# Kernel optimization log

Measured on AMD Instinct MI355X. Metric: run time of the kernel, lower is better.

The kernel has to match this reference:

```python
import jax, jax.numpy as jnp
import numpy as np

N_ATOMS = 50000
N_EDGES = 1_600_000
H = 128
EPS = 1e-3  # keras BatchNormalization default epsilon


def _bn(x, gamma, beta, mean, var):
    # inference-mode batch norm with moving statistics
    return gamma * (x - mean) * jax.lax.rsqrt(var + EPS) + beta


def setup_inputs() -> dict:
    key = jax.random.key(0)
    ks = jax.random.split(key, 16)
    s = 0.05
    D1 = H + 1
    inp = {
        "atom_embedding": jax.random.normal(ks[0], (N_ATOMS, H), jnp.float32),
        "bond_embedding": jax.random.normal(ks[1], (N_EDGES, H), jnp.float32),
        "indices_i": jax.random.randint(ks[2], (N_EDGES,), 0, N_ATOMS, dtype=jnp.int32),
        "indices_j": jax.random.randint(ks[3], (N_EDGES,), 0, N_ATOMS, dtype=jnp.int32),
        # preprocess: Dense(3H -> H+1, no bias) + BN, Dense(H+1 -> H+1, no bias) + BN
        "W1": jax.random.normal(ks[4], (3 * H, D1), jnp.float32) * s,
        "g1": jnp.ones((D1,), jnp.float32),
        "b1": jnp.zeros((D1,), jnp.float32),
        "m1": jnp.zeros((D1,), jnp.float32),
        "v1": jnp.ones((D1,), jnp.float32),
        "W2": jax.random.normal(ks[5], (D1, D1), jnp.float32) * s,
        "g2": jnp.ones((D1,), jnp.float32),
        "b2": jnp.zeros((D1,), jnp.float32),
        "m2": jnp.zeros((D1,), jnp.float32),
        "v2": jnp.ones((D1,), jnp.float32),
        # two residual layers, each: x + (x@w1+b1)@w2+b2 (activation=None)
        "r1w1": jax.random.normal(ks[6], (H, H), jnp.float32) * s,
        "r1b1": jnp.zeros((H,), jnp.float32),
        "r1w2": jax.random.normal(ks[7], (H, H), jnp.float32) * s,
        "r1b2": jnp.zeros((H,), jnp.float32),
        "r2w1": jax.random.normal(ks[8], (H, H), jnp.float32) * s,
        "r2b1": jnp.zeros((H,), jnp.float32),
        "r2w2": jax.random.normal(ks[9], (H, H), jnp.float32) * s,
        "r2b2": jnp.zeros((H,), jnp.float32),
    }
    return inp


def reference(atom_embedding, bond_embedding, indices_i, indices_j,
              W1, g1, b1, m1, v1, W2, g2, b2, m2, v2,
              r1w1, r1b1, r1w2, r1b2, r2w1, r2b1, r2w2, r2b2):
    # gather endpoints: [E, H]
    ai = atom_embedding[indices_i]
    aj = atom_embedding[indices_j]
    x = jnp.concatenate([ai, bond_embedding, aj], axis=-1)  # [E, 3H]
    x = _bn(x @ W1, g1, b1, m1, v1)  # [E, H+1]
    x = _bn(x @ W2, g2, b2, m2, v2)  # [E, H+1]
    msg = x[:, :1] * x[:, 1:]  # gate * message -> [E, H]
    atom = atom_embedding + jax.ops.segment_sum(msg, indices_i, num_segments=N_ATOMS)
    # residual MLPs (activation=None -> identity)
    atom = atom + (atom @ r1w1 + r1b1) @ r1w2 + r1b2
    atom = atom + (atom @ r2w1 + r2b1) @ r2w2 + r2b2
    return atom
```

## Files before the change

### kernel.cpp

```cpp
#include <hip/hip_runtime.h>

#define NA 50000
#define NE 1600000
#define HH 128
#define D1 129
#define EPS 1e-3f

typedef __bf16 bf16_t;
typedef bf16_t bf16x8 __attribute__((ext_vector_type(8)));
typedef bf16_t bf16x4 __attribute__((ext_vector_type(4)));
typedef float f32x4 __attribute__((ext_vector_type(4)));

#define OFF_A1   0
#define OFF_C1   129
#define OFF_A2   258
#define OFF_C2   387
#define OFF_WEFF 516
#define OFF_DVEC (OFF_WEFF + 384*129)
#define OFF_Q1   (OFF_DVEC + 129)
#define OFF_Q2   (OFF_Q1 + 128*128)
#define OFF_q1   (OFF_Q2 + 128*128)
#define OFF_q2   (OFF_q1 + 128)
#define OFF_QF   (OFF_q2 + 128)
#define OFF_qf   (OFF_QF + 128*128)
#define OFF_WMT  (((OFF_qf + 128) + 3) & ~3)
#define OFF_WTT  (OFF_WMT + 9216)
#define OFF_WBT  (OFF_WTT + 9216)
#define OFF_QFT  (OFF_WBT + 9216)
#define OFF_PI   (OFF_QFT + 8192)
#define OFF_PJ   (OFF_PI + NA*D1)
#define OFF_ACC  (OFF_PJ + NA*D1)
#define OFF_ACC2 (OFF_ACC + NA*HH)
#define OFF_CNT  (OFF_ACC2 + NA)
#define OFF_CUR  (OFF_CNT + NA)
#define OFF_EDG  (OFF_CUR + NA)
#define OFF_PART (OFF_EDG + NE)
#define OFF_IIS  (OFF_PART + 256)
#define OFF_JJS  (OFF_IIS + NE)
#define SCAN_NB  ((NA + 255) / 256)

__global__ void k_affine(const float* __restrict__ g1, const float* __restrict__ b1,
                         const float* __restrict__ m1, const float* __restrict__ v1,
                         const float* __restrict__ g2, const float* __restrict__ b2,
                         const float* __restrict__ m2, const float* __restrict__ v2,
                         float* __restrict__ ws) {
    for (int idx = threadIdx.x; idx < 2 * D1; idx += blockDim.x) {
        if (idx < D1) {
            float a = g1[idx] * rsqrtf(v1[idx] + EPS);
            ws[OFF_A1 + idx] = a;
            ws[OFF_C1 + idx] = b1[idx] - m1[idx] * a;
        } else {
            int n = idx - D1;
            float a = g2[n] * rsqrtf(v2[n] + EPS);
            ws[OFF_A2 + n] = a;
            ws[OFF_C2 + n] = b2[n] - m2[n] * a;
        }
    }
}

__global__ void k_weff(const float* __restrict__ W1, const float* __restrict__ W2,
                       float* __restrict__ ws) {
    int idx = blockIdx.x * blockDim.x + threadIdx.x;
    if (idx >= 384 * D1 + D1) return;
    const float* a1 = ws + OFF_A1;
    const float* c1 = ws + OFF_C1;
    const float* a2 = ws + OFF_A2;
    const float* c2 = ws + OFF_C2;
    if (idx < 384 * D1) {
        int k = idx / D1, n = idx % D1;
        float s = 0.f;
        for (int t = 0; t < D1; ++t)
            s += W1[(size_t)k * D1 + t] * a1[t] * W2[(size_t)t * D1 + n];
        ws[OFF_WEFF + idx] = s * a2[n];
    } else {
        int n = idx - 384 * D1;
        float s = 0.f;
        for (int t = 0; t < D1; ++t)
            s += c1[t] * W2[(size_t)t * D1 + n];
        ws[OFF_DVEC + n] = s * a2[n] + c2[n];
    }
}

__global__ void k_resid(const float* __restrict__ r1w1, const float* __restrict__ r1b1,
                        const float* __restrict__ r1w2, const float* __restrict__ r1b2,
                        const float* __restrict__ r2w1, const float* __restrict__ r2b1,
                        const float* __restrict__ r2w2, const float* __restrict__ r2b2,
                        float* __restrict__ ws) {
    int idx = blockIdx.x * blockDim.x + threadIdx.x;
    if (idx >= 2 * (128 * 128 + 128)) return;
    int layer = idx / (128 * 128 + 128);
    int r = idx % (128 * 128 + 128);
    const float* w1 = layer ? r2w1 : r1w1;
    const float* b1 = layer ? r2b1 : r1b1;
    const float* w2 = layer ? r2w2 : r1w2;
    const float* b2 = layer ? r2b2 : r1b2;
    float* Q = ws + (layer ? OFF_Q2 : OFF_Q1);
    float* q = ws + (layer ? OFF_q2 : OFF_q1);
    if (r < 128 * 128) {
        int i = r >> 7, j = r & 127;
        float s = (i == j) ? 1.f : 0.f;
        for (int t = 0; t < 128; ++t)
            s += w1[i * 128 + t] * w2[t * 128 + j];
        Q[r] = s;
    } else {
        int j = r - 128 * 128;
        float s = b2[j];
        for (int t = 0; t < 128; ++t)
            s += b1[t] * w2[t * 128 + j];
        q[j] = s;
    }
}

__global__ void k_qf(float* __restrict__ ws) {
    int idx = blockIdx.x * blockDim.x + threadIdx.x;
    if (idx >= 128 * 128 + 128) return;
    const float* Q1 = ws + OFF_Q1;
    const float* Q2 = ws + OFF_Q2;
    if (idx < 128 * 128) {
        int i = idx >> 7, j = idx & 127;
        float s = 0.f;
        for (int m = 0; m < 128; ++m)
            s += Q1[i * 128 + m] * Q2[m * 128 + j];
        ws[OFF_QF + idx] = s;
    } else {
        int j = idx - 128 * 128;
        const float* q1 = ws + OFF_q1;
        float s = ws[OFF_q2 + j];
        for (int m = 0; m < 128; ++m)
            s += q1[m] * Q2[m * 128 + j];
        ws[OFF_qf + j] = s;
    }
}

__global__ void k_pack(float* __restrict__ ws) {
    int idx = blockIdx.x * blockDim.x + threadIdx.x;
    const float* Weff = ws + OFF_WEFF;
    if (idx < 18432) {
        int n = idx >> 7, k = idx & 127;
        float v = (n < 128) ? Weff[(size_t)(128 + k) * D1 + n + 1]
                            : ((n == 128) ? Weff[(size_t)(128 + k) * D1] : 0.f);
        ((bf16_t*)(ws + OFF_WMT))[idx] = (bf16_t)v;
    } else if (idx < 2 * 18432) {
        int r = idx - 18432;
        int n = r >> 7, k = r & 127;
        float v = (n < D1) ? Weff[(size_t)k * D1 + n] : 0.f;
        ((bf16_t*)(ws + OFF_WTT))[r] = (bf16_t)v;
    } else if (idx < 3 * 18432) {
        int r = idx - 2 * 18432;
        int n = r >> 7, k = r & 127;
        float v = (n < D1) ? Weff[(size_t)(256 + k) * D1 + n] : 0.f;
        ((bf16_t*)(ws + OFF_WBT))[r] = (bf16_t)v;
    } else if (idx < 3 * 18432 + 16384) {
        int r = idx - 3 * 18432;
        int n = r >> 7, k = r & 127;
        ((bf16_t*)(ws + OFF_QFT))[r] = (bf16_t)ws[OFF_QF + k * 128 + n];
    }
}

__global__ void k_hist(const int* __restrict__ idx_i, float* __restrict__ ws) {
    int e = blockIdx.x * blockDim.x + threadIdx.x;
    if (e < NE) atomicAdd((int*)(ws + OFF_CNT) + idx_i[e], 1);
}

__global__ void k_scan1(float* __restrict__ ws) {
    const int* cnt = (const int*)(ws + OFF_CNT);
    int i = blockIdx.x * 256 + threadIdx.x;
    int v = (i < NA) ? cnt[i] : 0;
#pragma unroll
    for (int o = 1; o < 64; o <<= 1) v += __shfl_xor(v, o);
    __shared__ int wsum[4];
    if ((threadIdx.x & 63) == 0) wsum[threadIdx.x >> 6] = v;
    __syncthreads();
    if (threadIdx.x == 0)
        ((int*)(ws + OFF_PART))[blockIdx.x] = wsum[0] + wsum[1] + wsum[2] + wsum[3];
}

__global__ void k_scan2(float* __restrict__ ws) {
    int* part = (int*)(ws + OFF_PART);
    __shared__ int ps[256];
    int t = threadIdx.x;
    int v = (t < SCAN_NB) ? part[t] : 0;
    ps[t] = v;
    __syncthreads();
    for (int o = 1; o < 256; o <<= 1) {
        int u = (t >= o) ? ps[t - o] : 0;
        __syncthreads();
        ps[t] += u;
        __syncthreads();
    }
    part[t] = t ? ps[t - 1] : 0;
}

__global__ void k_scan3(float* __restrict__ ws) {
    const int* cnt = (const int*)(ws + OFF_CNT);
    int* cursor = (int*)(ws + OFF_CUR);
    int base = ((const int*)(ws + OFF_PART))[blockIdx.x];
    int i = blockIdx.x * 256 + threadIdx.x;
    int v = (i < NA) ? cnt[i] : 0;
    int lane = threadIdx.x & 63, w = threadIdx.x >> 6;
    int s = v;
#pragma unroll
    for (int o = 1; o < 64; o <<= 1) {
        int u = __shfl_up(s, o);
        if (lane >= o) s += u;
    }
    __shared__ int wtot[4];
    if (lane == 63) wtot[w] = s;
    __syncthreads();
    int add = 0;
    for (int k = 0; k < 4; ++k)
        if (k < w) add += wtot[k];
    if (i < NA) cursor[i] = base + add + s - v;
}

__global__ void k_scatter(const int* __restrict__ idx_i, const int* __restrict__ idx_j,
                          float* __restrict__ ws) {
    int e = blockIdx.x * blockDim.x + threadIdx.x;
    if (e < NE) {
        int i = idx_i[e];
        int p = atomicAdd((int*)(ws + OFF_CUR) + i, 1);
        ((int*)(ws + OFF_EDG))[p] = e;
        ((int*)(ws + OFF_IIS))[p] = i;
        ((int*)(ws + OFF_JJS))[p] = idx_j[e];
    }
}

__global__ __launch_bounds__(256) void k_gemm_mfma(
    const float* __restrict__ A, const float* __restrict__ A2,
    const float* __restrict__ Pi, const float* __restrict__ acc2,
    const bf16_t* __restrict__ Wt, const float* __restrict__ bias,
    float* __restrict__ C, int ldc, int N, int ntiles, int M) {
    __shared__ __align__(16) bf16_t As[64][136];
    int t = threadIdx.x;
    int m0 = blockIdx.x * 64;
#pragma unroll
    for (int it = 0; it < 8; ++it) {
        int idx = t + 256 * it;
        int r = idx >> 5, c4 = idx & 31;
        int grow = m0 + r;
        float4 v = make_float4(0.f, 0.f, 0.f, 0.f);
        if (grow < M) {
            v = ((const float4*)(A + (size_t)grow * 128))[c4];
            if (A2) {
                float4 w = ((const float4*)(A2 + (size_t)grow * 128))[c4];
                v.x += w.x; v.y += w.y; v.z += w.z; v.w += w.w;
            }
            if (acc2) {
                float s = acc2[grow];
                const float* p = Pi + (size_t)grow * D1 + 1 + c4 * 4;
                v.x += s * p[0]; v.y += s * p[1]; v.z += s * p[2]; v.w += s * p[3];
            }
        }
        bf16x4 tmp;
        tmp[0] = (bf16_t)v.x; tmp[1] = (bf16_t)v.y; tmp[2] = (bf16_t)v.z; tmp[3] = (bf16_t)v.w;
        *(bf16x4*)&As[r][c4 * 4] = tmp;
    }
    __syncthreads();
    int lane = t & 63, w = t >> 6;
    int ll = lane & 15, quad = lane >> 4;
    bf16x8 a[4];
#pragma unroll
    for (int k = 0; k < 4; ++k)
        a[k] = *(const bf16x8*)&As[w * 16 + ll][k * 32 + quad * 8];
    for (int nt = 0; nt < ntiles; ++nt) {
        const bf16_t* bp = Wt + (size_t)(nt * 16 + ll) * 128 + quad * 8;
        f32x4 acc = {0.f, 0.f, 0.f, 0.f};
#pragma unroll
        for (int k = 0; k < 4; ++k) {
            bf16x8 b = *(const bf16x8*)(bp + k * 32);
            acc = __builtin_amdgcn_mfma_f32_16x16x32_bf16(a[k], b, acc, 0, 0, 0);
        }
        int col = nt * 16 + ll;
        if (col < N) {
            float bv = bias ? bias[col] : 0.f;
#pragma unroll
            for (int r = 0; r < 4; ++r) {
                int row = m0 + w * 16 + quad * 4 + r;
                if (row < M) C[(size_t)row * ldc + col] = acc[r] + bv;
            }
        }
    }
}

__global__ __launch_bounds__(256) void k_pipj(
    const float* __restrict__ A, const bf16_t* __restrict__ Wt,
    const float* __restrict__ bias, float* __restrict__ Ct,
    const bf16_t* __restrict__ Wb, float* __restrict__ Cb, int M) {
    __shared__ __align__(16) bf16_t As[64][136];
    int t = threadIdx.x;
    int m0 = blockIdx.x * 64;
#pragma unroll
    for (int it = 0; it < 8; ++it) {
        int idx = t + 256 * it;
        int r = idx >> 5, c4 = idx & 31;
        int grow = m0 + r;
        float4 v = make_float4(0.f, 0.f, 0.f, 0.f);
        if (grow < M) v = ((const float4*)(A + (size_t)grow * 128))[c4];
        bf16x4 tmp;
        tmp[0] = (bf16_t)v.x; tmp[1] = (bf16_t)v.y; tmp[2] = (bf16_t)v.z; tmp[3] = (bf16_t)v.w;
        *(bf16x4*)&As[r][c4 * 4] = tmp;
    }
    __syncthreads();
    int lane = t & 63, w = t >> 6;
    int ll = lane & 15, quad = lane >> 4;
    bf16x8 a[4];
#pragma unroll
    for (int k = 0; k < 4; ++k)
        a[k] = *(const bf16x8*)&As[w * 16 + ll][k * 32 + quad * 8];
    for (int half = 0; half < 2; ++half) {
        const bf16_t* W = half ? Wb : Wt;
        float* C = half ? Cb : Ct;
        for (int nt = 0; nt < 9; ++nt) {
            const bf16_t* bp = W + (size_t)(nt * 16 + ll) * 128 + quad * 8;
            f32x4 acc = {0.f, 0.f, 0.f, 0.f};
#pragma unroll
            for (int k = 0; k < 4; ++k) {
                bf16x8 b = *(const bf16x8*)(bp + k * 32);
                acc = __builtin_amdgcn_mfma_f32_16x16x32_bf16(a[k], b, acc, 0, 0, 0);
            }
            int col = nt * 16 + ll;
            if (col < D1) {
                float bv = (half == 0 && bias) ? bias[col] : 0.f;
#pragma unroll
                for (int r = 0; r < 4; ++r) {
                    int row = m0 + w * 16 + quad * 4 + r;
                    if (row < M) C[(size_t)row * D1 + col] = acc[r] + bv;
                }
            }
        }
    }
}

__global__ __launch_bounds__(256, 3) void k_edge_mfma(
    const float* __restrict__ bond, const int* __restrict__ edge_of,
    const int* __restrict__ ii_srt, const int* __restrict__ jj_srt,
    const bf16_t* __restrict__ WmidT,
    const float* __restrict__ Pi, const float* __restrict__ Pj,
    float* __restrict__ accb, float* __restrict__ acc2) {
    __shared__ __align__(16) bf16_t As[2][64][136];

    int t = threadIdx.x;
    int lane = t & 63, w = t >> 6;
    int ll = lane & 15, quad = lane >> 4;
    size_t p0 = (size_t)blockIdx.x * 256;

    bf16x8 bg[4], bn0[4], bn1[4];
    {
        const bf16_t* gp = WmidT + (size_t)(128 + ll) * 128 + quad * 8;
        const bf16_t* q0 = WmidT + (size_t)(w * 32 + ll) * 128 + quad * 8;
        const bf16_t* q1 = WmidT + (size_t)(w * 32 + 16 + ll) * 128 + quad * 8;
#pragma unroll
        for (int k = 0; k < 4; ++k) {
            bg[k] = *(const bf16x8*)(gp + k * 32);
            bn0[k] = *(const bf16x8*)(q0 + k * 32);
            bn1[k] = *(const bf16x8*)(q1 + k * 32);
        }
    }
    int n0 = w * 32 + ll, n1 = w * 32 + 16 + ll;

    int mi = ii_srt[p0 + lane];
    int mj = jj_srt[p0 + lane];

#pragma unroll
    for (int it = 0; it < 8; ++it) {
        int idx = t + 256 * it;
        int r = idx >> 5, c4 = idx & 31;
        int e = edge_of[p0 + r];
        float4 v = ((const float4*)(bond + (size_t)e * 128))[c4];
        bf16x4 tmp;
        tmp[0] = (bf16_t)v.x; tmp[1] = (bf16_t)v.y; tmp[2] = (bf16_t)v.z; tmp[3] = (bf16_t)v.w;
        *(bf16x4*)&As[0][r][c4 * 4] = tmp;
    }
    __syncthreads();

    auto gather = [&](int smi, int smj, int eb2, float* p0v, float* p1v,
                      float* piv, float* pgv) {
#pragma unroll
        for (int r = 0; r < 4; ++r) {
            int jrr = __shfl(smj, eb2 + quad * 4 + r);
            int irr = __shfl(smi, eb2 + quad * 4 + r);
            const float* pjr = Pj + (size_t)jrr * D1;
            p0v[r] = pjr[1 + n0];
            p1v[r] = pjr[1 + n1];
            if (ll == 0) {
                piv[r] = Pi[(size_t)irr * D1];
                pgv[r] = pjr[0];
            }
        }
    };

    float pj0c[4], pj1c[4], pic[4], pjgc[4];
    gather(mi, mj, 0, pj0c, pj1c, pic, pjgc);

    for (int tt = 0; tt < 4; ++tt) {
        int buf = tt & 1;

        float4 pf[8];
        int nmi = 0, nmj = 0;
        if (tt < 3) {
            size_t nb = p0 + (size_t)(tt + 1) * 64;
#pragma unroll
            for (int it = 0; it < 8; ++it) {
                int idx = t + 256 * it;
                int r = idx >> 5, c4 = idx & 31;
                int e = edge_of[nb + r];
                pf[it] = ((const float4*)(bond + (size_t)e * 128))[c4];
            }
            nmi = ii_srt[nb + lane];
            nmj = jj_srt[nb + lane];
        }

#pragma unroll
        for (int g = 0; g < 4; ++g) {
            int eb = g * 16;
            bf16x8 a[4];
#pragma unroll
            for (int k = 0; k < 4; ++k)
                a[k] = *(const bf16x8*)&As[buf][eb + ll][k * 32 + quad * 8];

            int my = __shfl(mi, eb + ll);
            int pv = __shfl(mi, eb + (ll ? ll - 1 : 0));
            unsigned bmask = (unsigned)(__ballot(lane < 16 && ll > 0 && my != pv) & 0xFFFFull);

            float pj0n[4], pj1n[4], pin[4], pjgn[4];
            if (g < 3) gather(mi, mj, eb + 16, pj0n, pj1n, pin, pjgn);
            else if (tt < 3) gather(nmi, nmj, 0, pj0n, pj1n, pin, pjgn);

            f32x4 ag = {0.f, 0.f, 0.f, 0.f};
#pragma unroll
            for (int k = 0; k < 4; ++k)
                ag = __builtin_amdgcn_mfma_f32_16x16x32_bf16(a[k], bg[k], ag, 0, 0, 0);
            float gl[4];
#pragma unroll
            for (int r = 0; r < 4; ++r) {
                float v = ag[r];
                if (ll == 0) v += pic[r] + pjgc[r];
                gl[r] = __shfl(v, lane & 48);
            }

            if (w == 0) {
                int rs = 0;
                while (rs < 16) {
                    unsigned rest = bmask >> (rs + 1);
                    int re = rest ? rs + 1 + __builtin_ctz(rest) : 16;
                    float s = 0.f;
#pragma unroll
                    for (int r = 0; r < 4; ++r) {
                        int ee = quad * 4 + r;
                        if (ee >= rs && ee < re) s += gl[r];
                    }
                    s += __shfl_xor(s, 16);
                    s += __shfl_xor(s, 32);
                    int irs = __shfl(mi, eb + rs);
                    if (lane == 0) atomicAdd(&acc2[irs], s);
                    rs = re;
                }
            }

            f32x4 ac0 = {0.f, 0.f, 0.f, 0.f}, ac1 = {0.f, 0.f, 0.f, 0.f};
#pragma unroll
            for (int k = 0; k < 4; ++k)
                ac0 = __builtin_amdgcn_mfma_f32_16x16x32_bf16(a[k], bn0[k], ac0, 0, 0, 0);
#pragma unroll
            for (int k = 0; k < 4; ++k)
                ac1 = __builtin_amdgcn_mfma_f32_16x16x32_bf16(a[k], bn1[k], ac1, 0, 0, 0);
            float m0[4], m1[4];
#pragma unroll
            for (int r = 0; r < 4; ++r) {
                m0[r] = gl[r] * (ac0[r] + pj0c[r]);
                m1[r] = gl[r] * (ac1[r] + pj1c[r]);
            }

            int rs = 0;
            while (rs < 16) {
                unsigned rest = bmask >> (rs + 1);
                int re = rest ? rs + 1 + __builtin_ctz(rest) : 16;
                float s0 = 0.f, s1 = 0.f;
#pragma unroll
                for (int r = 0; r < 4; ++r) {
                    int ee = quad * 4 + r;
                    if (ee >= rs && ee < re) { s0 += m0[r]; s1 += m1[r]; }
                }
                s0 += __shfl_xor(s0, 16);
                s0 += __shfl_xor(s0, 32);
                s1 += __shfl_xor(s1, 16);
                s1 += __shfl_xor(s1, 32);
                int irs = __shfl(mi, eb + rs);
                if (quad == 0) {
                    float* ab = accb + (size_t)irs * 128;
                    atomicAdd(ab + n0, s0);
                    atomicAdd(ab + n1, s1);
                }
                rs = re;
            }

            if (g < 3 || tt < 3) {
#pragma unroll
                for (int r = 0; r < 4; ++r) {
                    pj0c[r] = pj0n[r]; pj1c[r] = pj1n[r];
                    pic[r] = pin[r];   pjgc[r] = pjgn[r];
                }
            }
        }

        if (tt < 3) {
            int nbuf = buf ^ 1;
#pragma unroll
            for (int it = 0; it < 8; ++it) {
                int idx = t + 256 * it;
                int r = idx >> 5, c4 = idx & 31;
                bf16x4 tmp;
                tmp[0] = (bf16_t)pf[it].x; tmp[1] = (bf16_t)pf[it].y;
                tmp[2] = (bf16_t)pf[it].z; tmp[3] = (bf16_t)pf[it].w;
                *(bf16x4*)&As[nbuf][r][c4 * 4] = tmp;
            }
            mi = nmi;
            mj = nmj;
        }
        __syncthreads();
    }
}

extern "C" void kernel_launch(void* const* d_in, const int* in_sizes, int n_in,
                              void* d_out, int out_size, void* d_ws, size_t ws_size,
                              hipStream_t stream) {
    const float* atom = (const float*)d_in[0];
    const float* bond = (const float*)d_in[1];
    const int* idx_i = (const int*)d_in[2];
    const int* idx_j = (const int*)d_in[3];
    const float* W1 = (const float*)d_in[4];
    const float* g1 = (const float*)d_in[5];
    const float* b1 = (const float*)d_in[6];
    const float* m1 = (const float*)d_in[7];
    const float* v1 = (const float*)d_in[8];
    const float* W2 = (const float*)d_in[9];
    const float* g2 = (const float*)d_in[10];
    const float* b2 = (const float*)d_in[11];
    const float* m2 = (const float*)d_in[12];
    const float* v2 = (const float*)d_in[13];
    const float* r1w1 = (const float*)d_in[14];
    const float* r1b1 = (const float*)d_in[15];
    const float* r1w2 = (const float*)d_in[16];
    const float* r1b2 = (const float*)d_in[17];
    const float* r2w1 = (const float*)d_in[18];
    const float* r2b1 = (const float*)d_in[19];
    const float* r2w2 = (const float*)d_in[20];
    const float* r2b2 = (const float*)d_in[21];
    float* ws = (float*)d_ws;
    float* out = (float*)d_out;

    hipMemsetAsync(ws + OFF_ACC, 0, (size_t)(NA * HH + 2 * NA) * sizeof(float), stream);

    k_hist<<<(NE + 255) / 256, 256, 0, stream>>>(idx_i, ws);
    k_scan1<<<SCAN_NB, 256, 0, stream>>>(ws);
    k_scan2<<<1, 256, 0, stream>>>(ws);
    k_scan3<<<SCAN_NB, 256, 0, stream>>>(ws);
    k_scatter<<<(NE + 255) / 256, 256, 0, stream>>>(idx_i, idx_j, ws);

    k_affine<<<1, 256, 0, stream>>>(g1, b1, m1, v1, g2, b2, m2, v2, ws);
    k_weff<<<(384 * D1 + D1 + 255) / 256, 256, 0, stream>>>(W1, W2, ws);
    k_resid<<<(2 * (128 * 128 + 128) + 255) / 256, 256, 0, stream>>>(
        r1w1, r1b1, r1w2, r1b2, r2w1, r2b1, r2w2, r2b2, ws);
    k_qf<<<(128 * 128 + 128 + 255) / 256, 256, 0, stream>>>(ws);
    k_pack<<<(3 * 18432 + 16384 + 255) / 256, 256, 0, stream>>>(ws);

    int gblocks = (NA + 63) / 64;
    k_pipj<<<gblocks, 256, 0, stream>>>(
        atom, (const bf16_t*)(ws + OFF_WTT), ws + OFF_DVEC, ws + OFF_PI,
        (const bf16_t*)(ws + OFF_WBT), ws + OFF_PJ, NA);

    k_edge_mfma<<<NE / 256, 256, 0, stream>>>(
        bond, (const int*)(ws + OFF_EDG), (const int*)(ws + OFF_IIS),
        (const int*)(ws + OFF_JJS), (const bf16_t*)(ws + OFF_WMT),
        ws + OFF_PI, ws + OFF_PJ, ws + OFF_ACC, ws + OFF_ACC2);

    k_gemm_mfma<<<gblocks, 256, 0, stream>>>(
        atom, ws + OFF_ACC, ws + OFF_PI, ws + OFF_ACC2, (const bf16_t*)(ws + OFF_QFT),
        ws + OFF_qf, out, 128, 128, 8, NA);
}
```

Measured before the change: 1.737 ms.

## Pack sorted i/j indices into one word, drop pack kernel, use nontemporal bond loads

```diff
diff --git a/kernel.cpp b/kernel.cpp
--- a/kernel.cpp
+++ b/kernel.cpp
@@ -35,9 +35,10 @@
 #define OFF_CUR  (OFF_CNT + NA)
 #define OFF_EDG  (OFF_CUR + NA)
 #define OFF_PART (OFF_EDG + NE)
-#define OFF_IIS  (OFF_PART + 256)
-#define OFF_JJS  (OFF_IIS + NE)
+#define OFF_IJS  (OFF_PART + 256)
 #define SCAN_NB  ((NA + 255) / 256)
+
+__device__ inline f32x4 ntload(const f32x4* p) { return __builtin_nontemporal_load(p); }
 
 __global__ void k_affine(const float* __restrict__ g1, const float* __restrict__ b1,
                          const float* __restrict__ m1, const float* __restrict__ v1,
@@ -56,6 +57,11 @@
             ws[OFF_C2 + n] = b2[n] - m2[n] * a;
         }
     }
+    for (int z = threadIdx.x; z < 3 * 960; z += blockDim.x) {
+        int arr = z / 960, off = z % 960;
+        float* base = ws + (arr == 0 ? OFF_WTT : (arr == 1 ? OFF_WMT : OFF_WBT));
+        ((unsigned*)base)[129 * 64 + off] = 0u;
+    }
 }
 
 __global__ void k_weff(const float* __restrict__ W1, const float* __restrict__ W2,
@@ -71,7 +77,16 @@
         float s = 0.f;
         for (int t = 0; t < D1; ++t)
             s += W1[(size_t)k * D1 + t] * a1[t] * W2[(size_t)t * D1 + n];
-        ws[OFF_WEFF + idx] = s * a2[n];
+        bf16_t b = (bf16_t)(s * a2[n]);
+        if (k < 128) {
+            ((bf16_t*)(ws + OFF_WTT))[n * 128 + k] = b;
+        } else if (k < 256) {
+            int kk = k - 128;
+            if (n == 0) ((bf16_t*)(ws + OFF_WMT))[128 * 128 + kk] = b;
+            else        ((bf16_t*)(ws + OFF_WMT))[(n - 1) * 128 + kk] = b;
+        } else {
+            ((bf16_t*)(ws + OFF_WBT))[n * 128 + (k - 256)] = b;
+        }
     } else {
         int n = idx - 384 * D1;
         float s = 0.f;
@@ -121,7 +136,7 @@
         float s = 0.f;
         for (int m = 0; m < 128; ++m)
             s += Q1[i * 128 + m] * Q2[m * 128 + j];
-        ws[OFF_QF + idx] = s;
+        ((bf16_t*)(ws + OFF_QFT))[j * 128 + i] = (bf16_t)s;
     } else {
         int j = idx - 128 * 128;
         const float* q1 = ws + OFF_q1;
@@ -129,31 +144,6 @@
         for (int m = 0; m < 128; ++m)
             s += q1[m] * Q2[m * 128 + j];
         ws[OFF_qf + j] = s;
-    }
-}
-
-__global__ void k_pack(float* __restrict__ ws) {
-    int idx = blockIdx.x * blockDim.x + threadIdx.x;
-    const float* Weff = ws + OFF_WEFF;
-    if (idx < 18432) {
-        int n = idx >> 7, k = idx & 127;
-        float v = (n < 128) ? Weff[(size_t)(128 + k) * D1 + n + 1]
-                            : ((n == 128) ? Weff[(size_t)(128 + k) * D1] : 0.f);
-        ((bf16_t*)(ws + OFF_WMT))[idx] = (bf16_t)v;
-    } else if (idx < 2 * 18432) {
-        int r = idx - 18432;
-        int n = r >> 7, k = r & 127;
-        float v = (n < D1) ? Weff[(size_t)k * D1 + n] : 0.f;
-        ((bf16_t*)(ws + OFF_WTT))[r] = (bf16_t)v;
-    } else if (idx < 3 * 18432) {
-        int r = idx - 2 * 18432;
-        int n = r >> 7, k = r & 127;
-        float v = (n < D1) ? Weff[(size_t)(256 + k) * D1 + n] : 0.f;
-        ((bf16_t*)(ws + OFF_WBT))[r] = (bf16_t)v;
-    } else if (idx < 3 * 18432 + 16384) {
-        int r = idx - 3 * 18432;
-        int n = r >> 7, k = r & 127;
-        ((bf16_t*)(ws + OFF_QFT))[r] = (bf16_t)ws[OFF_QF + k * 128 + n];
     }
 }
 
@@ -220,8 +210,7 @@
         int i = idx_i[e];
         int p = atomicAdd((int*)(ws + OFF_CUR) + i, 1);
         ((int*)(ws + OFF_EDG))[p] = e;
-        ((int*)(ws + OFF_IIS))[p] = i;
-        ((int*)(ws + OFF_JJS))[p] = idx_j[e];
+        ((unsigned*)(ws + OFF_IJS))[p] = ((unsigned)i << 16) | (unsigned)idx_j[e];
     }
 }
 
@@ -331,10 +320,9 @@
     }
 }
 
-__global__ __launch_bounds__(256, 3) void k_edge_mfma(
+__global__ __launch_bounds__(256, 4) void k_edge_mfma(
     const float* __restrict__ bond, const int* __restrict__ edge_of,
-    const int* __restrict__ ii_srt, const int* __restrict__ jj_srt,
-    const bf16_t* __restrict__ WmidT,
+    const unsigned* __restrict__ ij_srt, const bf16_t* __restrict__ WmidT,
     const float* __restrict__ Pi, const float* __restrict__ Pj,
     float* __restrict__ accb, float* __restrict__ acc2) {
     __shared__ __align__(16) bf16_t As[2][64][136];
@@ -356,47 +344,28 @@
             bn1[k] = *(const bf16x8*)(q1 + k * 32);
         }
     }
-    int n0 = w * 32 + ll, n1 = w * 32 + 16 + ll;
-
-    int mi = ii_srt[p0 + lane];
-    int mj = jj_srt[p0 + lane];
+    int n0 = w * 32 + ll, n1 = n0 + 16;
+
+    unsigned mij = ij_srt[p0 + lane];
 
 #pragma unroll
     for (int it = 0; it < 8; ++it) {
         int idx = t + 256 * it;
         int r = idx >> 5, c4 = idx & 31;
         int e = edge_of[p0 + r];
-        float4 v = ((const float4*)(bond + (size_t)e * 128))[c4];
+        f32x4 v = ntload((const f32x4*)(bond + (size_t)e * 128) + c4);
         bf16x4 tmp;
-        tmp[0] = (bf16_t)v.x; tmp[1] = (bf16_t)v.y; tmp[2] = (bf16_t)v.z; tmp[3] = (bf16_t)v.w;
+        tmp[0] = (bf16_t)v[0]; tmp[1] = (bf16_t)v[1];
+        tmp[2] = (bf16_t)v[2]; tmp[3] = (bf16_t)v[3];
         *(bf16x4*)&As[0][r][c4 * 4] = tmp;
     }
     __syncthreads();
-
-    auto gather = [&](int smi, int smj, int eb2, float* p0v, float* p1v,
-                      float* piv, float* pgv) {
-#pragma unroll
-        for (int r = 0; r < 4; ++r) {
-            int jrr = __shfl(smj, eb2 + quad * 4 + r);
-            int irr = __shfl(smi, eb2 + quad * 4 + r);
-            const float* pjr = Pj + (size_t)jrr * D1;
-            p0v[r] = pjr[1 + n0];
-            p1v[r] = pjr[1 + n1];
-            if (ll == 0) {
-                piv[r] = Pi[(size_t)irr * D1];
-                pgv[r] = pjr[0];
-            }
-        }
-    };
-
-    float pj0c[4], pj1c[4], pic[4], pjgc[4];
-    gather(mi, mj, 0, pj0c, pj1c, pic, pjgc);
 
     for (int tt = 0; tt < 4; ++tt) {
         int buf = tt & 1;
 
-        float4 pf[8];
-        int nmi = 0, nmj = 0;
+        f32x4 pf[8];
+        unsigned nmij = 0;
         if (tt < 3) {
             size_t nb = p0 + (size_t)(tt + 1) * 64;
 #pragma unroll
@@ -404,10 +373,9 @@
                 int idx = t + 256 * it;
                 int r = idx >> 5, c4 = idx & 31;
                 int e = edge_of[nb + r];
-                pf[it] = ((const float4*)(bond + (size_t)e * 128))[c4];
-            }
-            nmi = ii_srt[nb + lane];
-            nmj = jj_srt[nb + lane];
+                pf[it] = ntload((const f32x4*)(bond + (size_t)e * 128) + c4);
+            }
+            nmij = ij_srt[nb + lane];
         }
 
 #pragma unroll
@@ -418,13 +386,24 @@
             for (int k = 0; k < 4; ++k)
                 a[k] = *(const bf16x8*)&As[buf][eb + ll][k * 32 + quad * 8];
 
-            int my = __shfl(mi, eb + ll);
-            int pv = __shfl(mi, eb + (ll ? ll - 1 : 0));
-            unsigned bmask = (unsigned)(__ballot(lane < 16 && ll > 0 && my != pv) & 0xFFFFull);
-
-            float pj0n[4], pj1n[4], pin[4], pjgn[4];
-            if (g < 3) gather(mi, mj, eb + 16, pj0n, pj1n, pin, pjgn);
-            else if (tt < 3) gather(nmi, nmj, 0, pj0n, pj1n, pin, pjgn);
+            unsigned my = (unsigned)__shfl((int)mij, eb + ll);
+            unsigned pv = (unsigned)__shfl((int)mij, eb + (ll ? ll - 1 : 0));
+            unsigned bmask =
+                (unsigned)(__ballot(lane < 16 && ll > 0 && (my >> 16) != (pv >> 16)) & 0xFFFFull);
+
+            float pj0c[4], pj1c[4], pic[4], pjgc[4];
+            unsigned em[4];
+#pragma unroll
+            for (int r = 0; r < 4; ++r) {
+                em[r] = (unsigned)__shfl((int)mij, eb + quad * 4 + r);
+                const float* pjr = Pj + (size_t)(em[r] & 0xFFFFu) * D1;
+                pj0c[r] = pjr[1 + n0];
+                pj1c[r] = pjr[1 + n1];
+                if (ll == 0) {
+                    pic[r] = Pi[(size_t)(em[r] >> 16) * D1];
+                    pjgc[r] = pjr[0];
+                }
+            }
 
             f32x4 ag = {0.f, 0.f, 0.f, 0.f};
 #pragma unroll
@@ -451,7 +430,7 @@
                     }
                     s += __shfl_xor(s, 16);
                     s += __shfl_xor(s, 32);
-                    int irs = __shfl(mi, eb + rs);
+                    int irs = (int)(((unsigned)__shfl((int)mij, eb + rs)) >> 16);
                     if (lane == 0) atomicAdd(&acc2[irs], s);
                     rs = re;
                 }
@@ -485,7 +464,7 @@
                 s0 += __shfl_xor(s0, 32);
                 s1 += __shfl_xor(s1, 16);
                 s1 += __shfl_xor(s1, 32);
-                int irs = __shfl(mi, eb + rs);
+                int irs = (int)(((unsigned)__shfl((int)mij, eb + rs)) >> 16);
                 if (quad == 0) {
                     float* ab = accb + (size_t)irs * 128;
                     atomicAdd(ab + n0, s0);
@@ -493,14 +472,6 @@
                 }
                 rs = re;
             }
-
-            if (g < 3 || tt < 3) {
-#pragma unroll
-                for (int r = 0; r < 4; ++r) {
-                    pj0c[r] = pj0n[r]; pj1c[r] = pj1n[r];
-                    pic[r] = pin[r];   pjgc[r] = pjgn[r];
-                }
-            }
         }
 
         if (tt < 3) {
@@ -510,12 +481,11 @@
                 int idx = t + 256 * it;
                 int r = idx >> 5, c4 = idx & 31;
                 bf16x4 tmp;
-                tmp[0] = (bf16_t)pf[it].x; tmp[1] = (bf16_t)pf[it].y;
-                tmp[2] = (bf16_t)pf[it].z; tmp[3] = (bf16_t)pf[it].w;
+                tmp[0] = (bf16_t)pf[it][0]; tmp[1] = (bf16_t)pf[it][1];
+                tmp[2] = (bf16_t)pf[it][2]; tmp[3] = (bf16_t)pf[it][3];
                 *(bf16x4*)&As[nbuf][r][c4 * 4] = tmp;
             }
-            mi = nmi;
-            mj = nmj;
+            mij = nmij;
         }
         __syncthreads();
     }
@@ -562,7 +532,6 @@
     k_resid<<<(2 * (128 * 128 + 128) + 255) / 256, 256, 0, stream>>>(
         r1w1, r1b1, r1w2, r1b2, r2w1, r2b1, r2w2, r2b2, ws);
     k_qf<<<(128 * 128 + 128 + 255) / 256, 256, 0, stream>>>(ws);
-    k_pack<<<(3 * 18432 + 16384 + 255) / 256, 256, 0, stream>>>(ws);
 
     int gblocks = (NA + 63) / 64;
     k_pipj<<<gblocks, 256, 0, stream>>>(
@@ -570,8 +539,8 @@
         (const bf16_t*)(ws + OFF_WBT), ws + OFF_PJ, NA);
 
     k_edge_mfma<<<NE / 256, 256, 0, stream>>>(
-        bond, (const int*)(ws + OFF_EDG), (const int*)(ws + OFF_IIS),
-        (const int*)(ws + OFF_JJS), (const bf16_t*)(ws + OFF_WMT),
+        bond, (const int*)(ws + OFF_EDG), (const unsigned*)(ws + OFF_IJS),
+        (const bf16_t*)(ws + OFF_WMT),
         ws + OFF_PI, ws + OFF_PJ, ws + OFF_ACC, ws + OFF_ACC2);
 
     k_gemm_mfma<<<gblocks, 256, 0, stream>>>(
```

Result: no change. 1.720 ms (-0.9%).
